# Performance work log

Measured on AMD Instinct MI355X. Metric: run time of the kernel, lower is better.

Reference implementation:

```python
import jax, jax.numpy as jnp
import numpy as np


def setup_inputs() -> dict:
    N, E, D = 50000, 800000, 64
    key = jax.random.key(0)
    ks = jax.random.split(key, 8)
    s = 1.0 / np.sqrt(2 * D)
    inp = {
        "node_emb": jax.random.normal(ks[0], (N, D), dtype=jnp.float32),
        "edge_index": jax.random.randint(ks[1], (2, E), 0, N, dtype=jnp.int64),
        "W1": jax.random.normal(ks[2], (2 * D, D), dtype=jnp.float32) * s,
        "b1": jnp.zeros((D,), dtype=jnp.float32),
        "W2": jax.random.normal(ks[3], (D, D), dtype=jnp.float32) * (1.0 / np.sqrt(D)),
        "b2": jnp.zeros((D,), dtype=jnp.float32),
        "Wg": jax.random.normal(ks[4], (D, D), dtype=jnp.float32) * (1.0 / np.sqrt(D)),
        "bg": jnp.zeros((D,), dtype=jnp.float32),
    }
    return inp


def reference(node_emb, edge_index, W1, b1, W2, b2, Wg, bg):
    # Gather pairwise embeddings along edges
    src, dst = edge_index[0], edge_index[1]
    pair_emb = jnp.concatenate([node_emb[src], node_emb[dst]], axis=-1)  # [E, 2D]
    # Interaction MLP (dropout in eval mode -> identity)
    h = jax.nn.relu(pair_emb @ W1 + b1)
    interaction = h @ W2 + b2  # [E, D]
    # Sigmoid gate
    gate = jax.nn.sigmoid(interaction @ Wg + bg)
    gated = interaction * gate  # [E, D]
    # Scatter-mean back to source nodes
    N = node_emb.shape[0]
    summed = jax.ops.segment_sum(gated, src, num_segments=N)  # [N, D]
    counts = jax.ops.segment_sum(jnp.ones((src.shape[0],), dtype=gated.dtype), src, num_segments=N)
    pooled = summed / jnp.maximum(counts, 1.0)[:, None]
    return pooled
```

## Files before the change

### kernel.cpp

```cpp
#include <hip/hip_runtime.h>


typedef unsigned short ushort_t;
typedef __attribute__((ext_vector_type(8))) short     bf16x8;
typedef __attribute__((ext_vector_type(8))) unsigned short u16x8;
typedef __attribute__((ext_vector_type(4))) float     f32x4;

constexpr int D        = 64;
constexpr int TILE     = 64;
constexpr int BLOCK    = 256;
constexpr int NFRAG    = 32;
constexpr int SLAB_B   = 4352;
constexpr int PAIR_STR = 136;
constexpr int H_STR    = 72;

static __device__ __forceinline__ ushort_t f2bf(float f) {
    union { float f; unsigned int u; } v; v.f = f;
    const unsigned int r = v.u + 0x7FFFu + ((v.u >> 16) & 1u);
    return (ushort_t)(r >> 16);
}


__global__ void prep_kernel(const float* __restrict__ W1, const float* __restrict__ W2,
                            const float* __restrict__ Wg,
                            const float* __restrict__ b2, const float* __restrict__ bg,
                            const float* __restrict__ emb, const int* __restrict__ ei,
                            ushort_t* __restrict__ wpack, float* __restrict__ bgp,
                            ushort_t* __restrict__ emb_bf, int* __restrict__ cnt,
                            float* __restrict__ summed,
                            int total_emb, int cvt_blocks, int e4blocks, int E) {
    const int bid = blockIdx.x;
    if (bid < 64) {
        const int t = bid * 256 + threadIdx.x;
        const int f = t >> 9;
        const int l = (t >> 3) & 63;
        const int j = t & 7;
        const int k = ((f < 16) ? (f & 3) : ((f - 16) & 1)) * 32 + (l >> 4) * 8 + j;
        const int n = ((f < 16) ? (f >> 2) : (((f & 7)) >> 1)) * 16 + (l & 15);
        float v;
        if (f < 16)      v = W1[k * 64 + n];
        else if (f < 24) v = W2[k * 64 + n];
        else {
            float s = 0.f;
            const float* wr = W2 + k * 64;
#pragma unroll 8
            for (int m = 0; m < 64; ++m) s += wr[m] * Wg[m * 64 + n];
            v = s;
        }
        wpack[t] = f2bf(v);
    } else if (bid < 64 + cvt_blocks) {
        const int idx  = (bid - 64) * 256 + threadIdx.x;
        const int base = idx * 8;
        if (base < total_emb) {
            const float4 a = *(const float4*)(emb + base);
            const float4 b = *(const float4*)(emb + base + 4);
            u16x8 p;
            p[0]=f2bf(a.x); p[1]=f2bf(a.y); p[2]=f2bf(a.z); p[3]=f2bf(a.w);
            p[4]=f2bf(b.x); p[5]=f2bf(b.y); p[6]=f2bf(b.z); p[7]=f2bf(b.w);
            *(u16x8*)(emb_bf + base) = p;
        }
    } else if (bid == 64 + cvt_blocks) {
        const int n = threadIdx.x;
        if (n < 64) {
            float s = bg[n];
#pragma unroll 8
            for (int m = 0; m < 64; ++m) s += b2[m] * Wg[m * 64 + n];
            bgp[n] = s;
        }
    } else if (bid < 65 + cvt_blocks + e4blocks) {
        const int e = ((bid - 65 - cvt_blocks) * 256 + threadIdx.x) * 4;
        if (e + 3 < E) {
            const int4 v = *(const int4*)(ei + e);
            atomicAdd(&cnt[v.x], 1); atomicAdd(&cnt[v.y], 1);
            atomicAdd(&cnt[v.z], 1); atomicAdd(&cnt[v.w], 1);
        } else {
            for (int k = e; k < E; ++k) atomicAdd(&cnt[ei[k]], 1);
        }
    } else {
        const int idx  = (bid - 65 - cvt_blocks - e4blocks) * 256 + threadIdx.x;
        const int base = idx * 4;
        if (base < total_emb)
            *(float4*)(summed + base) = (float4){0.f, 0.f, 0.f, 0.f};
    }
}


__global__ void scan_block(const int* __restrict__ cnt, int* __restrict__ off,
                           int* __restrict__ bsum, int N) {
    __shared__ int s[256];
    const int t = threadIdx.x, i = blockIdx.x * 256 + t;
    const int x = (i < N) ? cnt[i] : 0;
    s[t] = x; __syncthreads();
    for (int d = 1; d < 256; d <<= 1) {
        const int v = (t >= d) ? s[t - d] : 0;
        __syncthreads();
        s[t] += v;
        __syncthreads();
    }
    if (i < N) off[i] = s[t] - x;
    if (t == 255) bsum[blockIdx.x] = s[255];
}

__global__ void scatter_idx(const int* __restrict__ ei, int* __restrict__ off,
                            const int* __restrict__ bsum, unsigned* __restrict__ sorted,
                            int E, int nb) {
    __shared__ int pref[256];
    const int t = threadIdx.x;
    const int x = (t < nb) ? bsum[t] : 0;
    pref[t] = x; __syncthreads();
    for (int d = 1; d < 256; d <<= 1) {
        const int v = (t >= d) ? pref[t - d] : 0;
        __syncthreads();
        pref[t] += v;
        __syncthreads();
    }
    const int e = (blockIdx.x * blockDim.x + t) * 4;
    if (e + 3 < E) {
        const int4 v = *(const int4*)(ei + e);
        const int4 d = *(const int4*)(ei + E + e);
        const int bx = v.x >> 8, by = v.y >> 8, bz = v.z >> 8, bw = v.w >> 8;
        sorted[(bx ? pref[bx - 1] : 0) + atomicAdd(&off[v.x], 1)] =
            ((unsigned)v.x << 16) | (unsigned)d.x;
        sorted[(by ? pref[by - 1] : 0) + atomicAdd(&off[v.y], 1)] =
            ((unsigned)v.y << 16) | (unsigned)d.y;
        sorted[(bz ? pref[bz - 1] : 0) + atomicAdd(&off[v.z], 1)] =
            ((unsigned)v.z << 16) | (unsigned)d.z;
        sorted[(bw ? pref[bw - 1] : 0) + atomicAdd(&off[v.w], 1)] =
            ((unsigned)v.w << 16) | (unsigned)d.w;
    } else {
        for (int k = e; k < E; ++k) {
            const int s = ei[k], b = s >> 8;
            sorted[(b ? pref[b - 1] : 0) + atomicAdd(&off[s], 1)] =
                ((unsigned)s << 16) | (unsigned)ei[E + k];
        }
    }
}


__global__ __launch_bounds__(BLOCK, 8)
void edge_mlp_mfma(const ushort_t* __restrict__ emb_bf,
                   const unsigned* __restrict__ sorted,
                   const ushort_t* __restrict__ wpack,
                   const float* __restrict__ b1, const float* __restrict__ b2,
                   const float* __restrict__ bgp,
                   const int*   __restrict__ cnt,
                   float* __restrict__ summed,
                   int E)
{
    __shared__ char  slab[4][SLAB_B];
    __shared__ int   srcIds[TILE];
    __shared__ float rcS[TILE];

    const int tid = threadIdx.x;

    {
        const int e = tid >> 2, q4 = tid & 3;
        ushort_t* prow = (ushort_t*)&slab[e >> 4][(e & 15) * (PAIR_STR * 2)];
        const int ide = blockIdx.x * TILE + e;
        if (ide < E) {
            const unsigned p = sorted[ide];
            const int s  = (int)(p >> 16);
            const int dn = (int)(p & 0xFFFFu);
            if (q4 == 0) { srcIds[e] = s; rcS[e] = 1.0f / fmaxf((float)cnt[s], 1.0f); }
            const ushort_t* sr = emb_bf + (size_t)s  * D + q4 * 16;
            const ushort_t* dr = emb_bf + (size_t)dn * D + q4 * 16;
            *(u16x8*)&prow[q4 * 16]          = *(const u16x8*)sr;
            *(u16x8*)&prow[q4 * 16 + 8]      = *(const u16x8*)(sr + 8);
            *(u16x8*)&prow[64 + q4 * 16]     = *(const u16x8*)dr;
            *(u16x8*)&prow[64 + q4 * 16 + 8] = *(const u16x8*)(dr + 8);
        } else {
            if (q4 == 0) { srcIds[e] = -1; rcS[e] = 1.0f; }
            const u16x8 z = {0,0,0,0,0,0,0,0};
            *(u16x8*)&prow[q4 * 16]          = z;
            *(u16x8*)&prow[q4 * 16 + 8]      = z;
            *(u16x8*)&prow[64 + q4 * 16]     = z;
            *(u16x8*)&prow[64 + q4 * 16 + 8] = z;
        }
    }

    const int w    = tid >> 6;
    const int ln   = tid & 63;
    const int quad = ln >> 4;
    const int cn   = ln & 15;
    ushort_t* pairW = (ushort_t*)slab[w];
    ushort_t* hW    = (ushort_t*)slab[w];

    f32x4 acc1[4];
#pragma unroll
    for (int nt = 0; nt < 4; ++nt) {
        const float b = b1[nt * 16 + cn];
        acc1[nt] = (f32x4){b, b, b, b};
    }
#pragma unroll
    for (int kc = 0; kc < 4; ++kc) {
        const bf16x8 a = *(const bf16x8*)&pairW[cn * PAIR_STR + kc * 32 + quad * 8];
#pragma unroll
        for (int nt = 0; nt < 4; ++nt) {
            const bf16x8 bf = *(const bf16x8*)(wpack + ((nt * 4 + kc) * 64 + ln) * 8);
            acc1[nt] = __builtin_amdgcn_mfma_f32_16x16x32_bf16(a, bf, acc1[nt], 0, 0, 0);
        }
    }
#pragma unroll
    for (int nt = 0; nt < 4; ++nt)
#pragma unroll
        for (int r = 0; r < 4; ++r)
            hW[(quad * 4 + r) * H_STR + nt * 16 + cn] = f2bf(fmaxf(acc1[nt][r], 0.f));

    f32x4 acc2[4], accg[4];
#pragma unroll
    for (int nt = 0; nt < 4; ++nt) {
        const float b  = b2 [nt * 16 + cn];
        const float bG = bgp[nt * 16 + cn];
        acc2[nt] = (f32x4){b, b, b, b};
        accg[nt] = (f32x4){bG, bG, bG, bG};
    }
#pragma unroll
    for (int kc = 0; kc < 2; ++kc) {
        const bf16x8 a = *(const bf16x8*)&hW[cn * H_STR + kc * 32 + quad * 8];
#pragma unroll
        for (int nt = 0; nt < 4; ++nt) {
            const bf16x8 bf2 = *(const bf16x8*)(wpack + ((16 + nt * 2 + kc) * 64 + ln) * 8);
            const bf16x8 bfg = *(const bf16x8*)(wpack + ((24 + nt * 2 + kc) * 64 + ln) * 8);
            acc2[nt] = __builtin_amdgcn_mfma_f32_16x16x32_bf16(a, bf2, acc2[nt], 0, 0, 0);
            accg[nt] = __builtin_amdgcn_mfma_f32_16x16x32_bf16(a, bfg, accg[nt], 0, 0, 0);
        }
    }

    float g[4][4];
#pragma unroll
    for (int nt = 0; nt < 4; ++nt)
#pragma unroll
        for (int r = 0; r < 4; ++r)
            g[nt][r] = acc2[nt][r] / (1.0f + __expf(-accg[nt][r]));

    {
        const int rbase = 16 * w;
        float part0 = 0.f, part1 = 0.f, part2 = 0.f, part3 = 0.f;
        int   segSrc = srcIds[rbase];
        int   segRow = 0;
#pragma unroll
        for (int i = 0; i < 16; ++i) {
            const int s = srcIds[rbase + i];
            if (s != segSrc) {
                if (segSrc >= 0) {
                    float t0 = part0, t1 = part1, t2 = part2, t3 = part3;
                    t0 += __shfl_xor(t0, 16); t0 += __shfl_xor(t0, 32);
                    t1 += __shfl_xor(t1, 16); t1 += __shfl_xor(t1, 32);
                    t2 += __shfl_xor(t2, 16); t2 += __shfl_xor(t2, 32);
                    t3 += __shfl_xor(t3, 16); t3 += __shfl_xor(t3, 32);
                    const float tot = (quad < 2) ? (quad == 0 ? t0 : t1)
                                                 : (quad == 2 ? t2 : t3);
                    unsafeAtomicAdd(&summed[(size_t)segSrc * D + ln],
                                    tot * rcS[rbase + segRow]);
                }
                part0 = part1 = part2 = part3 = 0.f;
                segSrc = s;
                segRow = i;
            }
            if ((i >> 2) == quad) {
                part0 += g[0][i & 3];
                part1 += g[1][i & 3];
                part2 += g[2][i & 3];
                part3 += g[3][i & 3];
            }
        }
        if (segSrc >= 0) {
            float t0 = part0, t1 = part1, t2 = part2, t3 = part3;
            t0 += __shfl_xor(t0, 16); t0 += __shfl_xor(t0, 32);
            t1 += __shfl_xor(t1, 16); t1 += __shfl_xor(t1, 32);
            t2 += __shfl_xor(t2, 16); t2 += __shfl_xor(t2, 32);
            t3 += __shfl_xor(t3, 16); t3 += __shfl_xor(t3, 32);
            const float tot = (quad < 2) ? (quad == 0 ? t0 : t1)
                                         : (quad == 2 ? t2 : t3);
            unsafeAtomicAdd(&summed[(size_t)segSrc * D + ln],
                            tot * rcS[rbase + segRow]);
        }
    }
}

extern "C" void kernel_launch(void* const* d_in, const int* in_sizes, int n_in,
                              void* d_out, int out_size, void* d_ws, size_t ws_size,
                              hipStream_t stream) {
    const float* node_emb   = (const float*)d_in[0];
    const int*   edge_index = (const int*)d_in[1];
    const float* W1 = (const float*)d_in[2];
    const float* b1 = (const float*)d_in[3];
    const float* W2 = (const float*)d_in[4];
    const float* b2 = (const float*)d_in[5];
    const float* Wg = (const float*)d_in[6];
    const float* bg = (const float*)d_in[7];

    const int N = in_sizes[0] / D;
    const int E = in_sizes[1] / 2;
    const int total_emb = N * D;

    int* cnt    = (int*)d_ws;
    int* off    = cnt + N;
    int* bsum   = off + N;
    unsigned* sorted = (unsigned*)(bsum + 256);
    float* bgp  = (float*)(sorted + E);
    ushort_t* wpack  = (ushort_t*)(bgp + 64);
    ushort_t* emb_bf = wpack + NFRAG * 512;

    float* summed = (float*)d_out;

    hipMemsetAsync(cnt, 0, sizeof(int) * (size_t)N, stream);

    const int cvt_blocks = (total_emb / 8 + 255) / 256;
    const int e4blocks   = ((E + 3) / 4 + 255) / 256;
    const int zblocks    = (total_emb / 4 + 255) / 256;
    prep_kernel<<<64 + cvt_blocks + 1 + e4blocks + zblocks, 256, 0, stream>>>(
        W1, W2, Wg, b2, bg, node_emb, edge_index,
        wpack, bgp, emb_bf, cnt, summed, total_emb, cvt_blocks, e4blocks, E);

    const int nblocks = (N + 255) / 256;
    scan_block <<<nblocks, 256, 0, stream>>>(cnt, off, bsum, N);
    scatter_idx<<<e4blocks, 256, 0, stream>>>(edge_index, off, bsum, sorted, E, nblocks);

    const int ntiles = (E + TILE - 1) / TILE;
    edge_mlp_mfma<<<ntiles, BLOCK, 0, stream>>>(emb_bf, sorted, wpack,
                                                b1, b2, bgp, cnt, summed, E);
}
```

Before: 244.8 us.

## Drop edge sort, scatter per-edge atomics, and divide by counts in a finalize pass

Removes the counting-sort pipeline (count, scan, scatter into a sorted index) and has the edge MLP read the edge_index directly. Each gated value is then atomically added to the output individually, counts are accumulated in the same kernel, and a new finalize kernel divides by the counts. The gate weights and bias are pre-scaled by log2(e), so the sigmoid uses the hardware exp2 and reciprocal instructions. This trades two launches and the sort traffic for many more uncoalesced float atomics, since segmented reduction over consecutive same-source edges is no longer possible.

New measurement: 297.2 us. +21.4%, slower.

```diff
diff --git a/kernel.cpp b/kernel.cpp
--- a/kernel.cpp
+++ b/kernel.cpp
@@ -13,6 +13,7 @@
 constexpr int SLAB_B   = 4352;
 constexpr int PAIR_STR = 136;
 constexpr int H_STR    = 72;
+constexpr float LOG2E  = 1.4426950408889634f;
 
 static __device__ __forceinline__ ushort_t f2bf(float f) {
     union { float f; unsigned int u; } v; v.f = f;
@@ -20,15 +21,22 @@
     return (ushort_t)(r >> 16);
 }
 
+static __device__ __forceinline__ float fexp2(float x) {
+    float r; asm("v_exp_f32 %0, %1" : "=v"(r) : "v"(x)); return r;
+}
+static __device__ __forceinline__ float frcp(float x) {
+    float r; asm("v_rcp_f32 %0, %1" : "=v"(r) : "v"(x)); return r;
+}
+
 
 __global__ void prep_kernel(const float* __restrict__ W1, const float* __restrict__ W2,
                             const float* __restrict__ Wg,
                             const float* __restrict__ b2, const float* __restrict__ bg,
-                            const float* __restrict__ emb, const int* __restrict__ ei,
+                            const float* __restrict__ emb,
                             ushort_t* __restrict__ wpack, float* __restrict__ bgp,
                             ushort_t* __restrict__ emb_bf, int* __restrict__ cnt,
                             float* __restrict__ summed,
-                            int total_emb, int cvt_blocks, int e4blocks, int E) {
+                            int total_emb, int N, int cvt_blocks, int zblocks) {
     const int bid = blockIdx.x;
     if (bid < 64) {
         const int t = bid * 256 + threadIdx.x;
@@ -45,7 +53,7 @@
             const float* wr = W2 + k * 64;
 #pragma unroll 8
             for (int m = 0; m < 64; ++m) s += wr[m] * Wg[m * 64 + n];
-            v = s;
+            v = s * LOG2E;
         }
         wpack[t] = f2bf(v);
     } else if (bid < 64 + cvt_blocks) {
@@ -65,73 +73,20 @@
             float s = bg[n];
 #pragma unroll 8
             for (int m = 0; m < 64; ++m) s += b2[m] * Wg[m * 64 + n];
-            bgp[n] = s;
-        }
-    } else if (bid < 65 + cvt_blocks + e4blocks) {
-        const int e = ((bid - 65 - cvt_blocks) * 256 + threadIdx.x) * 4;
-        if (e + 3 < E) {
-            const int4 v = *(const int4*)(ei + e);
-            atomicAdd(&cnt[v.x], 1); atomicAdd(&cnt[v.y], 1);
-            atomicAdd(&cnt[v.z], 1); atomicAdd(&cnt[v.w], 1);
-        } else {
-            for (int k = e; k < E; ++k) atomicAdd(&cnt[ei[k]], 1);
-        }
-    } else {
-        const int idx  = (bid - 65 - cvt_blocks - e4blocks) * 256 + threadIdx.x;
+            bgp[n] = s * LOG2E;
+        }
+    } else if (bid < 65 + cvt_blocks + zblocks) {
+        const int idx  = (bid - 65 - cvt_blocks) * 256 + threadIdx.x;
         const int base = idx * 4;
         if (base < total_emb)
             *(float4*)(summed + base) = (float4){0.f, 0.f, 0.f, 0.f};
-    }
-}
-
-
-__global__ void scan_block(const int* __restrict__ cnt, int* __restrict__ off,
-                           int* __restrict__ bsum, int N) {
-    __shared__ int s[256];
-    const int t = threadIdx.x, i = blockIdx.x * 256 + t;
-    const int x = (i < N) ? cnt[i] : 0;
-    s[t] = x; __syncthreads();
-    for (int d = 1; d < 256; d <<= 1) {
-        const int v = (t >= d) ? s[t - d] : 0;
-        __syncthreads();
-        s[t] += v;
-        __syncthreads();
-    }
-    if (i < N) off[i] = s[t] - x;
-    if (t == 255) bsum[blockIdx.x] = s[255];
-}
-
-__global__ void scatter_idx(const int* __restrict__ ei, int* __restrict__ off,
-                            const int* __restrict__ bsum, unsigned* __restrict__ sorted,
-                            int E, int nb) {
-    __shared__ int pref[256];
-    const int t = threadIdx.x;
-    const int x = (t < nb) ? bsum[t] : 0;
-    pref[t] = x; __syncthreads();
-    for (int d = 1; d < 256; d <<= 1) {
-        const int v = (t >= d) ? pref[t - d] : 0;
-        __syncthreads();
-        pref[t] += v;
-        __syncthreads();
-    }
-    const int e = (blockIdx.x * blockDim.x + t) * 4;
-    if (e + 3 < E) {
-        const int4 v = *(const int4*)(ei + e);
-        const int4 d = *(const int4*)(ei + E + e);
-        const int bx = v.x >> 8, by = v.y >> 8, bz = v.z >> 8, bw = v.w >> 8;
-        sorted[(bx ? pref[bx - 1] : 0) + atomicAdd(&off[v.x], 1)] =
-            ((unsigned)v.x << 16) | (unsigned)d.x;
-        sorted[(by ? pref[by - 1] : 0) + atomicAdd(&off[v.y], 1)] =
-            ((unsigned)v.y << 16) | (unsigned)d.y;
-        sorted[(bz ? pref[bz - 1] : 0) + atomicAdd(&off[v.z], 1)] =
-            ((unsigned)v.z << 16) | (unsigned)d.z;
-        sorted[(bw ? pref[bw - 1] : 0) + atomicAdd(&off[v.w], 1)] =
-            ((unsigned)v.w << 16) | (unsigned)d.w;
     } else {
-        for (int k = e; k < E; ++k) {
-            const int s = ei[k], b = s >> 8;
-            sorted[(b ? pref[b - 1] : 0) + atomicAdd(&off[s], 1)] =
-                ((unsigned)s << 16) | (unsigned)ei[E + k];
+        const int idx  = (bid - 65 - cvt_blocks - zblocks) * 256 + threadIdx.x;
+        const int base = idx * 4;
+        if (base + 3 < N) {
+            *(int4*)(cnt + base) = (int4){0, 0, 0, 0};
+        } else {
+            for (int k = base; k < N; ++k) cnt[k] = 0;
         }
     }
 }
@@ -139,17 +94,16 @@
 
 __global__ __launch_bounds__(BLOCK, 8)
 void edge_mlp_mfma(const ushort_t* __restrict__ emb_bf,
-                   const unsigned* __restrict__ sorted,
+                   const int* __restrict__ ei,
                    const ushort_t* __restrict__ wpack,
                    const float* __restrict__ b1, const float* __restrict__ b2,
                    const float* __restrict__ bgp,
-                   const int*   __restrict__ cnt,
+                   int*   __restrict__ cnt,
                    float* __restrict__ summed,
                    int E)
 {
     __shared__ char  slab[4][SLAB_B];
     __shared__ int   srcIds[TILE];
-    __shared__ float rcS[TILE];
 
     const int tid = threadIdx.x;
 
@@ -158,10 +112,9 @@
         ushort_t* prow = (ushort_t*)&slab[e >> 4][(e & 15) * (PAIR_STR * 2)];
         const int ide = blockIdx.x * TILE + e;
         if (ide < E) {
-            const unsigned p = sorted[ide];
-            const int s  = (int)(p >> 16);
-            const int dn = (int)(p & 0xFFFFu);
-            if (q4 == 0) { srcIds[e] = s; rcS[e] = 1.0f / fmaxf((float)cnt[s], 1.0f); }
+            const int s  = ei[ide];
+            const int dn = ei[E + ide];
+            if (q4 == 0) srcIds[e] = s;
             const ushort_t* sr = emb_bf + (size_t)s  * D + q4 * 16;
             const ushort_t* dr = emb_bf + (size_t)dn * D + q4 * 16;
             *(u16x8*)&prow[q4 * 16]          = *(const u16x8*)sr;
@@ -169,7 +122,7 @@
             *(u16x8*)&prow[64 + q4 * 16]     = *(const u16x8*)dr;
             *(u16x8*)&prow[64 + q4 * 16 + 8] = *(const u16x8*)(dr + 8);
         } else {
-            if (q4 == 0) { srcIds[e] = -1; rcS[e] = 1.0f; }
+            if (q4 == 0) srcIds[e] = -1;
             const u16x8 z = {0,0,0,0,0,0,0,0};
             *(u16x8*)&prow[q4 * 16]          = z;
             *(u16x8*)&prow[q4 * 16 + 8]      = z;
@@ -230,51 +183,36 @@
 #pragma unroll
     for (int nt = 0; nt < 4; ++nt)
 #pragma unroll
-        for (int r = 0; r < 4; ++r)
-            g[nt][r] = acc2[nt][r] / (1.0f + __expf(-accg[nt][r]));
-
-    {
-        const int rbase = 16 * w;
-        float part0 = 0.f, part1 = 0.f, part2 = 0.f, part3 = 0.f;
-        int   segSrc = srcIds[rbase];
-        int   segRow = 0;
-#pragma unroll
-        for (int i = 0; i < 16; ++i) {
-            const int s = srcIds[rbase + i];
-            if (s != segSrc) {
-                if (segSrc >= 0) {
-                    float t0 = part0, t1 = part1, t2 = part2, t3 = part3;
-                    t0 += __shfl_xor(t0, 16); t0 += __shfl_xor(t0, 32);
-                    t1 += __shfl_xor(t1, 16); t1 += __shfl_xor(t1, 32);
-                    t2 += __shfl_xor(t2, 16); t2 += __shfl_xor(t2, 32);
-                    t3 += __shfl_xor(t3, 16); t3 += __shfl_xor(t3, 32);
-                    const float tot = (quad < 2) ? (quad == 0 ? t0 : t1)
-                                                 : (quad == 2 ? t2 : t3);
-                    unsafeAtomicAdd(&summed[(size_t)segSrc * D + ln],
-                                    tot * rcS[rbase + segRow]);
-                }
-                part0 = part1 = part2 = part3 = 0.f;
-                segSrc = s;
-                segRow = i;
-            }
-            if ((i >> 2) == quad) {
-                part0 += g[0][i & 3];
-                part1 += g[1][i & 3];
-                part2 += g[2][i & 3];
-                part3 += g[3][i & 3];
-            }
-        }
-        if (segSrc >= 0) {
-            float t0 = part0, t1 = part1, t2 = part2, t3 = part3;
-            t0 += __shfl_xor(t0, 16); t0 += __shfl_xor(t0, 32);
-            t1 += __shfl_xor(t1, 16); t1 += __shfl_xor(t1, 32);
-            t2 += __shfl_xor(t2, 16); t2 += __shfl_xor(t2, 32);
-            t3 += __shfl_xor(t3, 16); t3 += __shfl_xor(t3, 32);
-            const float tot = (quad < 2) ? (quad == 0 ? t0 : t1)
-                                         : (quad == 2 ? t2 : t3);
-            unsafeAtomicAdd(&summed[(size_t)segSrc * D + ln],
-                            tot * rcS[rbase + segRow]);
-        }
+        for (int r = 0; r < 4; ++r) {
+            const float ex = fexp2(-accg[nt][r]);
+            g[nt][r] = acc2[nt][r] * frcp(1.0f + ex);
+        }
+
+#pragma unroll
+    for (int i = 0; i < 4; ++i) {
+        const int s = srcIds[16 * w + 4 * quad + i];
+        if (s >= 0) {
+            float* base = summed + (size_t)s * D + cn;
+            unsafeAtomicAdd(base,      g[0][i]);
+            unsafeAtomicAdd(base + 16, g[1][i]);
+            unsafeAtomicAdd(base + 32, g[2][i]);
+            unsafeAtomicAdd(base + 48, g[3][i]);
+            if (cn == 0) atomicAdd(&cnt[s], 1);
+        }
+    }
+}
+
+
+__global__ void finalize_kernel(float* __restrict__ summed, const int* __restrict__ cnt,
+                                int total_emb) {
+    const int idx  = blockIdx.x * 256 + threadIdx.x;
+    const int base = idx * 4;
+    if (base < total_emb) {
+        const int node = base >> 6;
+        const float rc = frcp(fmaxf((float)cnt[node], 1.0f));
+        float4 v = *(float4*)(summed + base);
+        v.x *= rc; v.y *= rc; v.z *= rc; v.w *= rc;
+        *(float4*)(summed + base) = v;
     }
 }
 
@@ -295,29 +233,22 @@
     const int total_emb = N * D;
 
     int* cnt    = (int*)d_ws;
-    int* off    = cnt + N;
-    int* bsum   = off + N;
-    unsigned* sorted = (unsigned*)(bsum + 256);
-    float* bgp  = (float*)(sorted + E);
+    float* bgp  = (float*)(cnt + N);
     ushort_t* wpack  = (ushort_t*)(bgp + 64);
     ushort_t* emb_bf = wpack + NFRAG * 512;
 
     float* summed = (float*)d_out;
 
-    hipMemsetAsync(cnt, 0, sizeof(int) * (size_t)N, stream);
-
     const int cvt_blocks = (total_emb / 8 + 255) / 256;
-    const int e4blocks   = ((E + 3) / 4 + 255) / 256;
     const int zblocks    = (total_emb / 4 + 255) / 256;
-    prep_kernel<<<64 + cvt_blocks + 1 + e4blocks + zblocks, 256, 0, stream>>>(
-        W1, W2, Wg, b2, bg, node_emb, edge_index,
-        wpack, bgp, emb_bf, cnt, summed, total_emb, cvt_blocks, e4blocks, E);
-
-    const int nblocks = (N + 255) / 256;
-    scan_block <<<nblocks, 256, 0, stream>>>(cnt, off, bsum, N);
-    scatter_idx<<<e4blocks, 256, 0, stream>>>(edge_index, off, bsum, sorted, E, nblocks);
+    const int cblocks    = ((N + 3) / 4 + 255) / 256;
+    prep_kernel<<<65 + cvt_blocks + zblocks + cblocks, 256, 0, stream>>>(
+        W1, W2, Wg, b2, bg, node_emb,
+        wpack, bgp, emb_bf, cnt, summed, total_emb, N, cvt_blocks, zblocks);
 
     const int ntiles = (E + TILE - 1) / TILE;
-    edge_mlp_mfma<<<ntiles, BLOCK, 0, stream>>>(emb_bf, sorted, wpack,
+    edge_mlp_mfma<<<ntiles, BLOCK, 0, stream>>>(emb_bf, edge_index, wpack,
                                                 b1, b2, bgp, cnt, summed, E);
-}
+
+    finalize_kernel<<<zblocks, 256, 0, stream>>>(summed, cnt, total_emb);
+}
```
